# Performance work log

Hardware: AMD Instinct MI355X
Metric: run time of the kernel (lower is better)

Reference implementation:

```python
import jax, jax.numpy as jnp
import numpy as np

DIM = 1024
HEADS = 16
HEAD_DIM = DIM // HEADS
B, T = 2, 2048


def setup_inputs() -> dict:
    key = jax.random.key(0)
    ks = jax.random.split(key, 6)
    x = jax.random.normal(ks[0], (B, T, DIM), dtype=jnp.float32)
    # Linear weights stored as [in, out] for x @ W + b
    w_qkv = jax.random.normal(ks[1], (DIM, 3 * DIM), dtype=jnp.float32) * (1.0 / np.sqrt(DIM))
    b_qkv = jnp.zeros((3 * DIM,), dtype=jnp.float32)
    w_out = jax.random.normal(ks[2], (DIM, DIM), dtype=jnp.float32) * (1.0 / np.sqrt(DIM))
    b_out = jnp.zeros((DIM,), dtype=jnp.float32)
    pos_bias = jax.random.normal(ks[3], (1, HEADS, 1, HEAD_DIM), dtype=jnp.float32) * 0.1
    return {"x": x, "w_qkv": w_qkv, "b_qkv": b_qkv, "w_out": w_out, "b_out": b_out, "pos_bias": pos_bias}


def reference(x, w_qkv, b_qkv, w_out, b_out, pos_bias):
    b, t, c = x.shape
    scale = HEAD_DIM ** -0.5
    qkv = x @ w_qkv + b_qkv                       # [B, T, 3C]
    q, k, v = jnp.split(qkv, 3, axis=-1)
    # [B, T, C] -> [B, H, T, Dh]
    def to_heads(z):
        return z.reshape(b, t, HEADS, HEAD_DIM).transpose(0, 2, 1, 3)
    q = to_heads(q) + pos_bias                    # learned query positional bias
    k = to_heads(k)
    v = to_heads(v)
    attn = jnp.einsum('bhqd,bhkd->bhqk', q, k) * scale
    causal = jnp.tril(jnp.ones((t, t), dtype=bool))
    attn = jnp.where(causal[None, None], attn, -jnp.inf)
    attn = jax.nn.softmax(attn, axis=-1)
    out = jnp.einsum('bhqk,bhkd->bhqd', attn, v)  # [B, H, T, Dh]
    out = out.transpose(0, 2, 1, 3).reshape(b, t, c)
    # dropout inactive (eval mode)
    return out @ w_out + b_out
```

## Files before the change

kernel.cpp:

```cpp
#include <hip/hip_runtime.h>

#define DIM 1024
#define HEADS 16
#define HD 64
#define BATCH 2
#define SEQ 2048
#define MROWS (BATCH*SEQ)
#define NQKV (3*DIM)
#define BK 32
#define ALDT 72

typedef unsigned short u16;
typedef __attribute__((ext_vector_type(8))) short short8;
typedef __attribute__((ext_vector_type(4))) float f32x4;

#define QSCALE 0.1803368801111204f

__device__ __forceinline__ u16 f2bf(float f) {
  unsigned u = __float_as_uint(f);
  u += 0x7FFFu + ((u >> 16) & 1u);
  return (u16)(u >> 16);
}

__device__ __forceinline__ void gload16(const u16* g, u16* l) {
  __builtin_amdgcn_global_load_lds((const __attribute__((address_space(1))) unsigned int*)g,
                                   (__attribute__((address_space(3))) unsigned int*)l, 16, 0, 0);
}

__global__ void k_f32_to_bf16(const float* __restrict__ in, u16* __restrict__ out, int n8) {
  int i = blockIdx.x * blockDim.x + threadIdx.x;
  if (i >= n8) return;
  const float4* p = (const float4*)in + (size_t)i * 2;
  float4 a = p[0], b = p[1];
  short8 v;
  v[0] = (short)f2bf(a.x); v[1] = (short)f2bf(a.y);
  v[2] = (short)f2bf(a.z); v[3] = (short)f2bf(a.w);
  v[4] = (short)f2bf(b.x); v[5] = (short)f2bf(b.y);
  v[6] = (short)f2bf(b.z); v[7] = (short)f2bf(b.w);
  ((short8*)out)[i] = v;
}

__global__ void k_transpose_f32_bf16(const float* __restrict__ in, u16* __restrict__ out,
                                     int R, int C) {
  __shared__ float tile[32][33];
  const int c0 = blockIdx.x * 32, r0 = blockIdx.y * 32;
  const int tx = threadIdx.x, ty = threadIdx.y;
#pragma unroll
  for (int i = 0; i < 4; ++i)
    tile[ty + 8 * i][tx] = in[(size_t)(r0 + ty + 8 * i) * C + c0 + tx];
  __syncthreads();
#pragma unroll
  for (int i = 0; i < 4; ++i)
    out[(size_t)(c0 + ty + 8 * i) * R + r0 + tx] = f2bf(tile[tx][ty + 8 * i]);
}

__global__ __launch_bounds__(256) void k_gemm_qkv(
    const u16* __restrict__ A, const u16* __restrict__ Bt,
    const float* __restrict__ bias, const float* __restrict__ posb,
    u16* __restrict__ qb, u16* __restrict__ kb, u16* __restrict__ vtb) {
  __shared__ u16 lA[128 * 32];
  __shared__ u16 lB[128 * 32];
  const int tid = threadIdx.x;
  const int lane = tid & 63;
  const int wid = tid >> 6;
  const int wm = wid >> 1, wn = wid & 1;
  const int rowA0 = blockIdx.y * 128;
  const int rowB0 = blockIdx.x * 128;
  const int rl = lane & 15, lg = lane >> 4;

  const f32x4 fz = {0.f, 0.f, 0.f, 0.f};
  f32x4 acc[4][4];
#pragma unroll
  for (int i = 0; i < 4; ++i)
#pragma unroll
    for (int j = 0; j < 4; ++j) acc[i][j] = fz;

  const int srow = tid >> 2;
  const int scol = ((tid & 3) ^ ((tid >> 3) & 3)) * 8;
  const u16* gA = A + (size_t)(rowA0 + srow) * DIM + scol;
  const u16* gB = Bt + (size_t)(rowB0 + srow) * DIM + scol;
  u16* dA0 = lA + tid * 8;
  u16* dA1 = lA + 2048 + tid * 8;
  u16* dB0 = lB + tid * 8;
  u16* dB1 = lB + 2048 + tid * 8;
  const int csw = (rl >> 1) & 3;

  for (int k0 = 0; k0 < DIM; k0 += BK) {
    __syncthreads();
    gload16(gA + k0, dA0);
    gload16(gA + (size_t)64 * DIM + k0, dA1);
    gload16(gB + k0, dB0);
    gload16(gB + (size_t)64 * DIM + k0, dB1);
    __syncthreads();
    short8 af[4], bfr[4];
#pragma unroll
    for (int mf = 0; mf < 4; ++mf)
      af[mf] = *(const short8*)(lA + (wm * 64 + mf * 16 + rl) * 32 + ((lg ^ csw) * 8));
#pragma unroll
    for (int nf = 0; nf < 4; ++nf)
      bfr[nf] = *(const short8*)(lB + (wn * 64 + nf * 16 + rl) * 32 + ((lg ^ csw) * 8));
#pragma unroll
    for (int mf = 0; mf < 4; ++mf)
#pragma unroll
      for (int nf = 0; nf < 4; ++nf)
        acc[mf][nf] = __builtin_amdgcn_mfma_f32_16x16x32_bf16(af[mf], bfr[nf], acc[mf][nf], 0, 0, 0);
  }

#pragma unroll
  for (int mf = 0; mf < 4; ++mf) {
#pragma unroll
    for (int nf = 0; nf < 4; ++nf) {
#pragma unroll
      for (int r = 0; r < 4; ++r) {
        const int row = rowA0 + wm * 64 + mf * 16 + lg * 4 + r;
        const int col = rowB0 + wn * 64 + nf * 16 + rl;
        float v = acc[mf][nf][r] + bias[col];
        const int which = col >> 10;
        const int within = col & 1023;
        const int h = within >> 6, d = within & 63;
        const int bb = row >> 11, t = row & 2047;
        const size_t bh = (size_t)(bb * HEADS + h);
        if (which == 0) {
          v = (v + posb[within]) * QSCALE;
          qb[(bh * SEQ + t) * HD + d] = f2bf(v);
        } else if (which == 1) {
          kb[(bh * SEQ + t) * HD + d] = f2bf(v);
        } else {
          vtb[(bh * HD + d) * SEQ + t] = f2bf(v);
        }
      }
    }
  }
}

__global__ __launch_bounds__(256) void k_attn(
    const u16* __restrict__ qg, const u16* __restrict__ kg, const u16* __restrict__ vg,
    u16* __restrict__ og) {
  __shared__ u16 lK[64 * ALDT];
  __shared__ u16 lV[64 * ALDT];
  const int tid = threadIdx.x;
  const int lane = tid & 63;
  const int wid = tid >> 6;
  const int rl = lane & 15, lg = lane >> 4;
  const int pair = blockIdx.x & 15;
  const int bh = blockIdx.x >> 4;
  const int b = bh >> 4, h = bh & 15;

  const u16* gK = kg + (size_t)bh * SEQ * HD;
  const u16* gV = vg + (size_t)bh * HD * SEQ;
  const int sr = tid >> 3;
  const int sc = (tid & 7) * 8;
  const int sl0 = (((2 * lg) & 3) << 4) + rl;
  const int sl1 = (((2 * lg + 1) & 3) << 4) + rl;
  const bool hi = (lg >= 2);

#pragma unroll 1
  for (int half = 0; half < 2; ++half) {
    const int qt = half ? pair : (31 - pair);
    const int qrow = qt * 64 + wid * 16 + rl;
    const u16* qptr = qg + ((size_t)bh * SEQ + qrow) * HD + lg * 8;
    const short8 aq0 = *(const short8*)(qptr);
    const short8 aq1 = *(const short8*)(qptr + 32);

    const f32x4 fz = {0.f, 0.f, 0.f, 0.f};
    f32x4 o[4];
#pragma unroll
    for (int dt = 0; dt < 4; ++dt) o[dt] = fz;
    float m = -1e30f, l = 0.f;

    int4 rka = *(const int4*)(gK + (size_t)sr * HD + sc);
    int4 rkb = *(const int4*)(gK + (size_t)(sr + 32) * HD + sc);
    int4 rva = *(const int4*)(gV + (size_t)sr * SEQ + sc);
    int4 rvb = *(const int4*)(gV + (size_t)(sr + 32) * SEQ + sc);

    for (int kt = 0; kt <= qt; ++kt) {
      __syncthreads();
      *(int4*)(lK + sr * ALDT + sc) = rka;
      *(int4*)(lK + (sr + 32) * ALDT + sc) = rkb;
      *(int4*)(lV + sr * ALDT + sc) = rva;
      *(int4*)(lV + (sr + 32) * ALDT + sc) = rvb;
      __syncthreads();
      if (kt < qt) {
        const int kv1 = (kt + 1) * 64;
        rka = *(const int4*)(gK + (size_t)(kv1 + sr) * HD + sc);
        rkb = *(const int4*)(gK + (size_t)(kv1 + sr + 32) * HD + sc);
        rva = *(const int4*)(gV + (size_t)sr * SEQ + kv1 + sc);
        rvb = *(const int4*)(gV + (size_t)(sr + 32) * SEQ + kv1 + sc);
      }

      f32x4 s[4];
#pragma unroll
      for (int ct = 0; ct < 4; ++ct) s[ct] = fz;
#pragma unroll
      for (int ct = 0; ct < 4; ++ct) {
        short8 ak0 = *(const short8*)(lK + (ct * 16 + rl) * ALDT + lg * 8);
        short8 ak1 = *(const short8*)(lK + (ct * 16 + rl) * ALDT + 32 + lg * 8);
        s[ct] = __builtin_amdgcn_mfma_f32_16x16x32_bf16(ak0, aq0, s[ct], 0, 0, 0);
        s[ct] = __builtin_amdgcn_mfma_f32_16x16x32_bf16(ak1, aq1, s[ct], 0, 0, 0);
      }

      if (kt == qt) {
#pragma unroll
        for (int ct = 0; ct < 4; ++ct)
#pragma unroll
          for (int r = 0; r < 4; ++r)
            if (kt * 64 + ct * 16 + lg * 4 + r > qrow) s[ct][r] = -1e30f;
      }

      float pmax = -1e30f;
#pragma unroll
      for (int ct = 0; ct < 4; ++ct)
#pragma unroll
        for (int r = 0; r < 4; ++r) pmax = fmaxf(pmax, s[ct][r]);
      pmax = fmaxf(pmax, __shfl_xor(pmax, 16, 64));
      pmax = fmaxf(pmax, __shfl_xor(pmax, 32, 64));
      const float mn = fmaxf(m, pmax);
      const float alpha = __builtin_amdgcn_exp2f(m - mn);
      m = mn;
      float rs = 0.f;
      unsigned pk[4][2];
#pragma unroll
      for (int ct = 0; ct < 4; ++ct) {
        float p0 = __builtin_amdgcn_exp2f(s[ct][0] - mn);
        float p1 = __builtin_amdgcn_exp2f(s[ct][1] - mn);
        float p2 = __builtin_amdgcn_exp2f(s[ct][2] - mn);
        float p3 = __builtin_amdgcn_exp2f(s[ct][3] - mn);
        rs += (p0 + p1) + (p2 + p3);
        pk[ct][0] = (unsigned)f2bf(p0) | ((unsigned)f2bf(p1) << 16);
        pk[ct][1] = (unsigned)f2bf(p2) | ((unsigned)f2bf(p3) << 16);
      }
      l = l * alpha + rs;
#pragma unroll
      for (int dt = 0; dt < 4; ++dt)
#pragma unroll
        for (int r = 0; r < 4; ++r) o[dt][r] *= alpha;

#pragma unroll
      for (int kb2 = 0; kb2 < 2; ++kb2) {
        unsigned a0 = (unsigned)__shfl((int)pk[2 * kb2 + 0][0], sl0, 64);
        unsigned b0 = (unsigned)__shfl((int)pk[2 * kb2 + 1][0], sl0, 64);
        unsigned a1 = (unsigned)__shfl((int)pk[2 * kb2 + 0][1], sl0, 64);
        unsigned b1 = (unsigned)__shfl((int)pk[2 * kb2 + 1][1], sl0, 64);
        unsigned a2 = (unsigned)__shfl((int)pk[2 * kb2 + 0][0], sl1, 64);
        unsigned b2 = (unsigned)__shfl((int)pk[2 * kb2 + 1][0], sl1, 64);
        unsigned a3 = (unsigned)__shfl((int)pk[2 * kb2 + 0][1], sl1, 64);
        unsigned b3 = (unsigned)__shfl((int)pk[2 * kb2 + 1][1], sl1, 64);
        union { unsigned u[4]; short8 s8; } pu;
        pu.u[0] = hi ? b0 : a0;
        pu.u[1] = hi ? b1 : a1;
        pu.u[2] = hi ? b2 : a2;
        pu.u[3] = hi ? b3 : a3;
#pragma unroll
        for (int dt = 0; dt < 4; ++dt) {
          short8 av = *(const short8*)(lV + (dt * 16 + rl) * ALDT + kb2 * 32 + lg * 8);
          o[dt] = __builtin_amdgcn_mfma_f32_16x16x32_bf16(av, pu.s8, o[dt], 0, 0, 0);
        }
      }
    }

    l += __shfl_xor(l, 16, 64);
    l += __shfl_xor(l, 32, 64);
    const float linv = __builtin_amdgcn_rcpf(l);
    const size_t obase = ((size_t)b * SEQ + qrow) * DIM + h * HD;
#pragma unroll
    for (int dt = 0; dt < 4; ++dt) {
      union { u16 e[4]; uint2 v; } w;
      w.e[0] = f2bf(o[dt][0] * linv);
      w.e[1] = f2bf(o[dt][1] * linv);
      w.e[2] = f2bf(o[dt][2] * linv);
      w.e[3] = f2bf(o[dt][3] * linv);
      *(uint2*)(og + obase + dt * 16 + lg * 4) = w.v;
    }
  }
}

__global__ __launch_bounds__(256) void k_gemm_out(
    const u16* __restrict__ A, const u16* __restrict__ Bt,
    const float* __restrict__ bias, float* __restrict__ out) {
  __shared__ u16 lA[128 * 32];
  __shared__ u16 lB[128 * 32];
  const int tid = threadIdx.x;
  const int lane = tid & 63;
  const int wid = tid >> 6;
  const int wm = wid >> 1, wn = wid & 1;
  const int rowA0 = blockIdx.y * 128;
  const int rowB0 = blockIdx.x * 128;
  const int rl = lane & 15, lg = lane >> 4;

  const f32x4 fz = {0.f, 0.f, 0.f, 0.f};
  f32x4 acc[4][4];
#pragma unroll
  for (int i = 0; i < 4; ++i)
#pragma unroll
    for (int j = 0; j < 4; ++j) acc[i][j] = fz;

  const int srow = tid >> 2;
  const int scol = ((tid & 3) ^ ((tid >> 3) & 3)) * 8;
  const u16* gA = A + (size_t)(rowA0 + srow) * DIM + scol;
  const u16* gB = Bt + (size_t)(rowB0 + srow) * DIM + scol;
  u16* dA0 = lA + tid * 8;
  u16* dA1 = lA + 2048 + tid * 8;
  u16* dB0 = lB + tid * 8;
  u16* dB1 = lB + 2048 + tid * 8;
  const int csw = (rl >> 1) & 3;

  for (int k0 = 0; k0 < DIM; k0 += BK) {
    __syncthreads();
    gload16(gA + k0, dA0);
    gload16(gA + (size_t)64 * DIM + k0, dA1);
    gload16(gB + k0, dB0);
    gload16(gB + (size_t)64 * DIM + k0, dB1);
    __syncthreads();
    short8 af[4], bfr[4];
#pragma unroll
    for (int mf = 0; mf < 4; ++mf)
      af[mf] = *(const short8*)(lA + (wm * 64 + mf * 16 + rl) * 32 + ((lg ^ csw) * 8));
#pragma unroll
    for (int nf = 0; nf < 4; ++nf)
      bfr[nf] = *(const short8*)(lB + (wn * 64 + nf * 16 + rl) * 32 + ((lg ^ csw) * 8));
#pragma unroll
    for (int mf = 0; mf < 4; ++mf)
#pragma unroll
      for (int nf = 0; nf < 4; ++nf)
        acc[mf][nf] = __builtin_amdgcn_mfma_f32_16x16x32_bf16(af[mf], bfr[nf], acc[mf][nf], 0, 0, 0);
  }

#pragma unroll
  for (int mf = 0; mf < 4; ++mf)
#pragma unroll
    for (int nf = 0; nf < 4; ++nf)
#pragma unroll
      for (int r = 0; r < 4; ++r) {
        const int row = rowA0 + wm * 64 + mf * 16 + lg * 4 + r;
        const int col = rowB0 + wn * 64 + nf * 16 + rl;
        out[(size_t)row * DIM + col] = acc[mf][nf][r] + bias[col];
      }
}

extern "C" void kernel_launch(void* const* d_in, const int* in_sizes, int n_in,
                              void* d_out, int out_size, void* d_ws, size_t ws_size,
                              hipStream_t stream) {
  const float* x = (const float*)d_in[0];
  const float* w_qkv = (const float*)d_in[1];
  const float* b_qkv = (const float*)d_in[2];
  const float* w_out = (const float*)d_in[3];
  const float* b_out = (const float*)d_in[4];
  const float* pos_bias = (const float*)d_in[5];
  float* out = (float*)d_out;

  u16* ws = (u16*)d_ws;
  u16* xb = ws;
  u16* wqkvb = xb + (size_t)MROWS * DIM;
  u16* woutb = wqkvb + (size_t)NQKV * DIM;
  u16* qb = woutb + (size_t)DIM * DIM;
  u16* kbuf = qb + (size_t)BATCH * HEADS * SEQ * HD;
  u16* vtb = kbuf + (size_t)BATCH * HEADS * SEQ * HD;
  u16* attnb = xb;

  k_f32_to_bf16<<<(MROWS * DIM / 8 + 255) / 256, 256, 0, stream>>>(x, xb, MROWS * DIM / 8);
  k_transpose_f32_bf16<<<dim3(NQKV / 32, DIM / 32), dim3(32, 8), 0, stream>>>(w_qkv, wqkvb, DIM, NQKV);
  k_transpose_f32_bf16<<<dim3(DIM / 32, DIM / 32), dim3(32, 8), 0, stream>>>(w_out, woutb, DIM, DIM);
  k_gemm_qkv<<<dim3(NQKV / 128, MROWS / 128), 256, 0, stream>>>(xb, wqkvb, b_qkv, pos_bias, qb, kbuf, vtb);
  k_attn<<<dim3(BATCH * HEADS * 16), 256, 0, stream>>>(qb, kbuf, vtb, attnb);
  k_gemm_out<<<dim3(DIM / 128, MROWS / 128), 256, 0, stream>>>(attnb, woutb, b_out, out);
}
```

Baseline: 229.0 us.

## Triple-buffer GEMM LDS loads and raise wave priority around attention MFMAs

Both projection GEMMs switch from a single LDS buffer with two barriers per k-step to a three-stage ring, fed by async global-to-LDS loads issued two tiles ahead with vmcnt-based waits and a single barrier per step. This is meant to hide global load latency behind the MFMA work. The attention kernel also wraps its QK and PV MFMA blocks in s_setprio to favour matrix issue across waves. LDS per GEMM block grows to 48KB, which may lower occupancy.

```diff
diff --git a/kernel.cpp b/kernel.cpp
--- a/kernel.cpp
+++ b/kernel.cpp
@@ -8,6 +8,7 @@
 #define MROWS (BATCH*SEQ)
 #define NQKV (3*DIM)
 #define BK 32
+#define NT (DIM/BK)
 #define ALDT 72
 
 typedef unsigned short u16;
@@ -54,57 +55,71 @@
     out[(size_t)(c0 + ty + 8 * i) * R + r0 + tx] = f2bf(tile[tx][ty + 8 * i]);
 }
 
+#define GEMM_PREAMBLE(Aptr, Bptr)                                              \
+  __shared__ u16 lds_[3 * 8192];                                               \
+  const int tid = threadIdx.x;                                                 \
+  const int lane = tid & 63;                                                   \
+  const int wid = tid >> 6;                                                    \
+  const int wm = wid >> 1, wn = wid & 1;                                       \
+  const int rowA0 = blockIdx.y * 128;                                          \
+  const int rowB0 = blockIdx.x * 128;                                          \
+  const int rl = lane & 15, lg = lane >> 4;                                    \
+  const int csw = (rl >> 1) & 3;                                               \
+  const f32x4 fz = {0.f, 0.f, 0.f, 0.f};                                       \
+  f32x4 acc[4][4];                                                             \
+  _Pragma("unroll") for (int i = 0; i < 4; ++i)                                \
+  _Pragma("unroll") for (int j = 0; j < 4; ++j) acc[i][j] = fz;                \
+  const int srow = tid >> 2;                                                   \
+  const int scol = ((tid & 3) ^ ((tid >> 3) & 3)) * 8;                         \
+  const u16* gA = (Aptr) + (size_t)(rowA0 + srow) * DIM + scol;                \
+  const u16* gB = (Bptr) + (size_t)(rowB0 + srow) * DIM + scol;                \
+  auto stage = [&](int t, int j) {                                             \
+    u16* d = lds_ + j * 8192;                                                  \
+    gload16(gA + t * BK, d + tid * 8);                                         \
+    gload16(gA + (size_t)64 * DIM + t * BK, d + 2048 + tid * 8);               \
+    gload16(gB + t * BK, d + 4096 + tid * 8);                                  \
+    gload16(gB + (size_t)64 * DIM + t * BK, d + 6144 + tid * 8);               \
+  };                                                                           \
+  auto compute = [&](int j) {                                                  \
+    const u16* bufA = lds_ + j * 8192;                                         \
+    const u16* bufB = bufA + 4096;                                             \
+    short8 af[4], bfr[4];                                                      \
+    _Pragma("unroll") for (int mf = 0; mf < 4; ++mf)                           \
+      af[mf] = *(const short8*)(bufA + (wm * 64 + mf * 16 + rl) * 32 +         \
+                                ((lg ^ csw) * 8));                             \
+    _Pragma("unroll") for (int nf = 0; nf < 4; ++nf)                           \
+      bfr[nf] = *(const short8*)(bufB + (wn * 64 + nf * 16 + rl) * 32 +        \
+                                 ((lg ^ csw) * 8));                            \
+    _Pragma("unroll") for (int mf = 0; mf < 4; ++mf)                           \
+    _Pragma("unroll") for (int nf = 0; nf < 4; ++nf)                           \
+      acc[mf][nf] =                                                            \
+          __builtin_amdgcn_mfma_f32_16x16x32_bf16(af[mf], bfr[nf],             \
+                                                  acc[mf][nf], 0, 0, 0);       \
+  };                                                                           \
+  stage(0, 0);                                                                 \
+  stage(1, 1);                                                                 \
+  asm volatile("s_waitcnt vmcnt(4)" ::: "memory");                             \
+  __builtin_amdgcn_s_barrier();                                                \
+  int cur = 0;                                                                 \
+  _Pragma("unroll 3") for (int t = 0; t < NT - 2; ++t) {                       \
+    int nb = cur + 2; if (nb >= 3) nb -= 3;                                    \
+    stage(t + 2, nb);                                                          \
+    compute(cur);                                                              \
+    asm volatile("s_waitcnt vmcnt(4)" ::: "memory");                           \
+    __builtin_amdgcn_s_barrier();                                              \
+    cur = cur + 1; if (cur == 3) cur = 0;                                      \
+  }                                                                            \
+  compute(cur);                                                                \
+  asm volatile("s_waitcnt vmcnt(0)" ::: "memory");                             \
+  __builtin_amdgcn_s_barrier();                                                \
+  cur = cur + 1; if (cur == 3) cur = 0;                                        \
+  compute(cur);
+
 __global__ __launch_bounds__(256) void k_gemm_qkv(
     const u16* __restrict__ A, const u16* __restrict__ Bt,
     const float* __restrict__ bias, const float* __restrict__ posb,
     u16* __restrict__ qb, u16* __restrict__ kb, u16* __restrict__ vtb) {
-  __shared__ u16 lA[128 * 32];
-  __shared__ u16 lB[128 * 32];
-  const int tid = threadIdx.x;
-  const int lane = tid & 63;
-  const int wid = tid >> 6;
-  const int wm = wid >> 1, wn = wid & 1;
-  const int rowA0 = blockIdx.y * 128;
-  const int rowB0 = blockIdx.x * 128;
-  const int rl = lane & 15, lg = lane >> 4;
-
-  const f32x4 fz = {0.f, 0.f, 0.f, 0.f};
-  f32x4 acc[4][4];
-#pragma unroll
-  for (int i = 0; i < 4; ++i)
-#pragma unroll
-    for (int j = 0; j < 4; ++j) acc[i][j] = fz;
-
-  const int srow = tid >> 2;
-  const int scol = ((tid & 3) ^ ((tid >> 3) & 3)) * 8;
-  const u16* gA = A + (size_t)(rowA0 + srow) * DIM + scol;
-  const u16* gB = Bt + (size_t)(rowB0 + srow) * DIM + scol;
-  u16* dA0 = lA + tid * 8;
-  u16* dA1 = lA + 2048 + tid * 8;
-  u16* dB0 = lB + tid * 8;
-  u16* dB1 = lB + 2048 + tid * 8;
-  const int csw = (rl >> 1) & 3;
-
-  for (int k0 = 0; k0 < DIM; k0 += BK) {
-    __syncthreads();
-    gload16(gA + k0, dA0);
-    gload16(gA + (size_t)64 * DIM + k0, dA1);
-    gload16(gB + k0, dB0);
-    gload16(gB + (size_t)64 * DIM + k0, dB1);
-    __syncthreads();
-    short8 af[4], bfr[4];
-#pragma unroll
-    for (int mf = 0; mf < 4; ++mf)
-      af[mf] = *(const short8*)(lA + (wm * 64 + mf * 16 + rl) * 32 + ((lg ^ csw) * 8));
-#pragma unroll
-    for (int nf = 0; nf < 4; ++nf)
-      bfr[nf] = *(const short8*)(lB + (wn * 64 + nf * 16 + rl) * 32 + ((lg ^ csw) * 8));
-#pragma unroll
-    for (int mf = 0; mf < 4; ++mf)
-#pragma unroll
-      for (int nf = 0; nf < 4; ++nf)
-        acc[mf][nf] = __builtin_amdgcn_mfma_f32_16x16x32_bf16(af[mf], bfr[nf], acc[mf][nf], 0, 0, 0);
-  }
+  GEMM_PREAMBLE(A, Bt)
 
 #pragma unroll
   for (int mf = 0; mf < 4; ++mf) {
@@ -133,6 +148,23 @@
   }
 }
 
+__global__ __launch_bounds__(256) void k_gemm_out(
+    const u16* __restrict__ A, const u16* __restrict__ Bt,
+    const float* __restrict__ bias, float* __restrict__ out) {
+  GEMM_PREAMBLE(A, Bt)
+
+#pragma unroll
+  for (int mf = 0; mf < 4; ++mf)
+#pragma unroll
+    for (int nf = 0; nf < 4; ++nf)
+#pragma unroll
+      for (int r = 0; r < 4; ++r) {
+        const int row = rowA0 + wm * 64 + mf * 16 + lg * 4 + r;
+        const int col = rowB0 + wn * 64 + nf * 16 + rl;
+        out[(size_t)row * DIM + col] = acc[mf][nf][r] + bias[col];
+      }
+}
+
 __global__ __launch_bounds__(256) void k_attn(
     const u16* __restrict__ qg, const u16* __restrict__ kg, const u16* __restrict__ vg,
     u16* __restrict__ og) {
@@ -191,6 +223,7 @@
       f32x4 s[4];
 #pragma unroll
       for (int ct = 0; ct < 4; ++ct) s[ct] = fz;
+      __builtin_amdgcn_s_setprio(1);
 #pragma unroll
       for (int ct = 0; ct < 4; ++ct) {
         short8 ak0 = *(const short8*)(lK + (ct * 16 + rl) * ALDT + lg * 8);
@@ -198,6 +231,7 @@
         s[ct] = __builtin_amdgcn_mfma_f32_16x16x32_bf16(ak0, aq0, s[ct], 0, 0, 0);
         s[ct] = __builtin_amdgcn_mfma_f32_16x16x32_bf16(ak1, aq1, s[ct], 0, 0, 0);
       }
+      __builtin_amdgcn_s_setprio(0);
 
       if (kt == qt) {
 #pragma unroll
@@ -250,11 +284,13 @@
         pu.u[1] = hi ? b1 : a1;
         pu.u[2] = hi ? b2 : a2;
         pu.u[3] = hi ? b3 : a3;
+        __builtin_amdgcn_s_setprio(1);
 #pragma unroll
         for (int dt = 0; dt < 4; ++dt) {
           short8 av = *(const short8*)(lV + (dt * 16 + rl) * ALDT + kb2 * 32 + lg * 8);
           o[dt] = __builtin_amdgcn_mfma_f32_16x16x32_bf16(av, pu.s8, o[dt], 0, 0, 0);
         }
+        __builtin_amdgcn_s_setprio(0);
       }
     }
 
@@ -272,69 +308,6 @@
       *(uint2*)(og + obase + dt * 16 + lg * 4) = w.v;
     }
   }
-}
-
-__global__ __launch_bounds__(256) void k_gemm_out(
-    const u16* __restrict__ A, const u16* __restrict__ Bt,
-    const float* __restrict__ bias, float* __restrict__ out) {
-  __shared__ u16 lA[128 * 32];
-  __shared__ u16 lB[128 * 32];
-  const int tid = threadIdx.x;
-  const int lane = tid & 63;
-  const int wid = tid >> 6;
-  const int wm = wid >> 1, wn = wid & 1;
-  const int rowA0 = blockIdx.y * 128;
-  const int rowB0 = blockIdx.x * 128;
-  const int rl = lane & 15, lg = lane >> 4;
-
-  const f32x4 fz = {0.f, 0.f, 0.f, 0.f};
-  f32x4 acc[4][4];
-#pragma unroll
-  for (int i = 0; i < 4; ++i)
-#pragma unroll
-    for (int j = 0; j < 4; ++j) acc[i][j] = fz;
-
-  const int srow = tid >> 2;
-  const int scol = ((tid & 3) ^ ((tid >> 3) & 3)) * 8;
-  const u16* gA = A + (size_t)(rowA0 + srow) * DIM + scol;
-  const u16* gB = Bt + (size_t)(rowB0 + srow) * DIM + scol;
-  u16* dA0 = lA + tid * 8;
-  u16* dA1 = lA + 2048 + tid * 8;
-  u16* dB0 = lB + tid * 8;
-  u16* dB1 = lB + 2048 + tid * 8;
-  const int csw = (rl >> 1) & 3;
-
-  for (int k0 = 0; k0 < DIM; k0 += BK) {
-    __syncthreads();
-    gload16(gA + k0, dA0);
-    gload16(gA + (size_t)64 * DIM + k0, dA1);
-    gload16(gB + k0, dB0);
-    gload16(gB + (size_t)64 * DIM + k0, dB1);
-    __syncthreads();
-    short8 af[4], bfr[4];
-#pragma unroll
-    for (int mf = 0; mf < 4; ++mf)
-      af[mf] = *(const short8*)(lA + (wm * 64 + mf * 16 + rl) * 32 + ((lg ^ csw) * 8));
-#pragma unroll
-    for (int nf = 0; nf < 4; ++nf)
-      bfr[nf] = *(const short8*)(lB + (wn * 64 + nf * 16 + rl) * 32 + ((lg ^ csw) * 8));
-#pragma unroll
-    for (int mf = 0; mf < 4; ++mf)
-#pragma unroll
-      for (int nf = 0; nf < 4; ++nf)
-        acc[mf][nf] = __builtin_amdgcn_mfma_f32_16x16x32_bf16(af[mf], bfr[nf], acc[mf][nf], 0, 0, 0);
-  }
-
-#pragma unroll
-  for (int mf = 0; mf < 4; ++mf)
-#pragma unroll
-    for (int nf = 0; nf < 4; ++nf)
-#pragma unroll
-      for (int r = 0; r < 4; ++r) {
-        const int row = rowA0 + wm * 64 + mf * 16 + lg * 4 + r;
-        const int col = rowB0 + wn * 64 + nf * 16 + rl;
-        out[(size_t)row * DIM + col] = acc[mf][nf][r] + bias[col];
-      }
 }
 
 extern "C" void kernel_launch(void* const* d_in, const int* in_sizes, int n_in,
```

New measurement: 200.9 us. -12.3%, faster.
